# Kernel optimization log

Measured on AMD Instinct MI355X. Metric: run time of the kernel, lower is better.

The kernel has to match this reference:

```python
import jax, jax.numpy as jnp
import numpy as np

# Constants mirroring privacy_config
LEAK = 0.95          # membrane_leak_rate
REFR = 2.0           # refractory_period
SYN_EPS = 0.1        # synaptic_epsilon (threshold noise scale & privacy-cost factor)
NOISE_SCALE = 0.05   # spike_noise_scale on inputs
THRESH = 1.0         # spike_threshold init
SIZES = [1024, 2048, 1024, 512]
T, B = 16, 256


def setup_inputs() -> dict:
    key = jax.random.key(0)
    ks = jax.random.split(key, 16)
    inp = {"inputs": jax.random.normal(ks[0], (B, SIZES[0]), dtype=jnp.float32)}
    for i in range(3):
        nin, nout = SIZES[i], SIZES[i + 1]
        inp[f"w{i}"] = jax.random.normal(ks[1 + i], (nout, nin), dtype=jnp.float32) * 0.1
        inp[f"th{i}"] = jnp.full((nout,), THRESH, dtype=jnp.float32)
        inp[f"cn{i}"] = jax.random.normal(ks[4 + i], (T, B, nout), dtype=jnp.float32)
        inp[f"tn{i}"] = jax.random.normal(ks[7 + i], (T, B, nout), dtype=jnp.float32)
    inp["time_steps"] = T
    return inp


def _forward(inputs, ws, ths, cns, tns):
    # Vectorized leaky integrate-and-fire across (batch, neuron), scanned over time.
    Bsz = inputs.shape[0]
    Tn = cns[0].shape[0]
    nL = len(ws)
    V0 = tuple(jnp.zeros((Bsz, w.shape[0]), inputs.dtype) for w in ws)
    ls0 = tuple(jnp.full((Bsz, w.shape[0]), -1e9, inputs.dtype) for w in ws)  # last spike time
    wnorms = [jnp.linalg.norm(w, axis=1) for w in ws]  # per-neuron weight-vector norm [N]
    times = jnp.arange(1, Tn + 1, dtype=inputs.dtype)

    def step(carry, xs):
        t, cn_t, tn_t = xs
        Vs, ls = carry
        act = inputs  # input is re-presented at each time step (layer_activities[0])
        nV, nls, sps = [], [], []
        for i in range(nL):
            # per-neuron input noise ~ N(0, scale^2) dotted with w -> N(0, scale^2*||w||^2)
            cur = act @ ws[i].T + cn_t[i] * (NOISE_SCALE * wnorms[i])  # [B, N]
            refrac = (t - ls[i]) < REFR  # refractory neurons skip the update entirely
            Vn = jnp.where(refrac, Vs[i], LEAK * Vs[i] + cur)
            thr = ths[i] + tn_t[i] * SYN_EPS  # noisy privacy threshold
            sp = jnp.logical_and(jnp.logical_not(refrac), Vn > thr)
            nV.append(jnp.where(sp, 0.0, Vn))         # reset membrane on spike
            nls.append(jnp.where(sp, t, ls[i]))
            act = sp.astype(inputs.dtype)              # spikes feed next layer
            sps.append(act)
        return (tuple(nV), tuple(nls)), tuple(sps)

    _, spikes = jax.lax.scan(step, (V0, ls0), (times, tuple(cns), tuple(tns)))
    # spikes: tuple of [T, B, N_l] per layer

    # privacy cost: eps * (spikes in trailing 10-step window)/10 * ||w_neuron||, summed over all calls
    idx = jnp.arange(Tn)
    idx_hi = idx + 1
    idx_lo = jnp.clip(idx - 9, 0, Tn)
    cost = jnp.zeros((), inputs.dtype)
    tot = jnp.zeros((), inputs.dtype)
    cnt = 0
    for sp, wn in zip(spikes, wnorms):
        cs = jnp.concatenate([jnp.zeros_like(sp[:1]), jnp.cumsum(sp, axis=0)], axis=0)
        win = cs[idx_hi] - cs[idx_lo]  # [T, B, N] trailing-window spike counts
        cost = cost + SYN_EPS * jnp.sum(win / 10.0 * wn)
        tot = tot + jnp.sum(sp)
        cnt += sp.size
    # network entropy over the binary {0,1} spike pattern values
    p1 = tot / cnt
    p0 = 1.0 - p1
    eps = 1e-12
    entropy = -(p1 * jnp.log2(p1 + eps) + p0 * jnp.log2(p0 + eps))

    out = spikes[-1][-1]  # last layer activity at final time step, [B, N_last]
    return out, cost, entropy


def reference(inputs, w0, w1, w2, th0, th1, th2, cn0, cn1, cn2, tn0, tn1, tn2, time_steps):
    return _forward(inputs, (w0, w1, w2), (th0, th1, th2), (cn0, cn1, cn2), (tn0, tn1, tn2))
```

## Files before the change

kernel.cpp:

```cpp
#include <hip/hip_runtime.h>
#include <math.h>


#define T_STEPS 16

typedef short short8 __attribute__((ext_vector_type(8)));
typedef float floatx4 __attribute__((ext_vector_type(4)));

__device__ inline ushort f2bf(float x) {
  unsigned int u = __float_as_uint(x);
  unsigned int r = (u + 0x7FFFu + ((u >> 16) & 1u)) >> 16;
  return (ushort)r;
}
__device__ inline float bf2f(ushort h) {
  return __uint_as_float(((unsigned int)h) << 16);
}
__device__ inline floatx4 mfma16(short8 a, short8 b, floatx4 c) {
  return __builtin_amdgcn_mfma_f32_16x16x32_bf16(a, b, c, 0, 0, 0);
}

__device__ inline void gload16(const ushort* g, ushort* l) {
  __builtin_amdgcn_global_load_lds(
      (const __attribute__((address_space(1))) void*)g,
      (__attribute__((address_space(3))) void*)l, 16, 0, 0);
}

__device__ inline void stage_split16(const float* __restrict__ src, ushort* dsth, ushort* dstl) {
  float fv[16];
  #pragma unroll
  for (int i = 0; i < 4; ++i) *(float4*)&fv[4 * i] = *(const float4*)(src + 4 * i);
  unsigned int ph[8], pl[8];
  #pragma unroll
  for (int i = 0; i < 8; ++i) {
    ushort h0 = f2bf(fv[2 * i]);
    ushort l0 = f2bf(fv[2 * i] - bf2f(h0));
    ushort h1 = f2bf(fv[2 * i + 1]);
    ushort l1 = f2bf(fv[2 * i + 1] - bf2f(h1));
    ph[i] = (unsigned int)h0 | ((unsigned int)h1 << 16);
    pl[i] = (unsigned int)l0 | ((unsigned int)l1 << 16);
  }
  *(uint4*)dsth       = make_uint4(ph[0], ph[1], ph[2], ph[3]);
  *(uint4*)(dsth + 8) = make_uint4(ph[4], ph[5], ph[6], ph[7]);
  *(uint4*)dstl       = make_uint4(pl[0], pl[1], pl[2], pl[3]);
  *(uint4*)(dstl + 8) = make_uint4(pl[4], pl[5], pl[6], pl[7]);
}

__device__ inline void cost_store_bucket(float csum, int cnt, float2* __restrict__ cbuf,
                                         int bucket_base) {
  #pragma unroll
  for (int off = 32; off > 0; off >>= 1) {
    csum += __shfl_down(csum, off);
    cnt  += __shfl_down(cnt, off);
  }
  __shared__ float sc[4];
  __shared__ int   si[4];
  int wid = threadIdx.x >> 6;
  if ((threadIdx.x & 63) == 0) { sc[wid] = csum; si[wid] = cnt; }
  __syncthreads();
  if (threadIdx.x == 0) {
    float c = sc[0] + sc[1] + sc[2] + sc[3];
    int   k = si[0] + si[1] + si[2] + si[3];
    float2 v;
    v.x = c * 0.01f;
    v.y = (float)k;
    cbuf[bucket_base + blockIdx.x] = v;
  }
}


__global__ __launch_bounds__(64) void wnorm_kernel(const float* __restrict__ w0,
                                                   const float* __restrict__ w1,
                                                   const float* __restrict__ w2,
                                                   float* __restrict__ wn) {
  int r = blockIdx.x;
  const float* row; int K;
  if (r < 2048)      { row = w0 + (size_t)r * 1024;          K = 1024; }
  else if (r < 3072) { row = w1 + (size_t)(r - 2048) * 2048; K = 2048; }
  else               { row = w2 + (size_t)(r - 3072) * 1024; K = 1024; }
  float ss = 0.f;
  for (int k = threadIdx.x; k < K; k += 64) { float x = row[k]; ss += x * x; }
  #pragma unroll
  for (int off = 32; off > 0; off >>= 1) ss += __shfl_down(ss, off);
  if (threadIdx.x == 0) wn[r] = sqrtf(ss);
}


__global__ __launch_bounds__(256) void convert_w_kernel(const float* __restrict__ w1,
                                                        const float* __restrict__ w2,
                                                        ushort* __restrict__ w1b,
                                                        ushort* __restrict__ w2b) {
  int i = (blockIdx.x * 256 + threadIdx.x) * 8;
  const float* src; ushort* dst;
  if (i < 2097152) { src = w1 + i; dst = w1b + i; }
  else             { src = w2 + (i - 2097152); dst = w2b + (i - 2097152); }
  float4 a = *(const float4*)src;
  float4 b = *(const float4*)(src + 4);
  unsigned int p0 = (unsigned int)f2bf(a.x) | ((unsigned int)f2bf(a.y) << 16);
  unsigned int p1 = (unsigned int)f2bf(a.z) | ((unsigned int)f2bf(a.w) << 16);
  unsigned int p2 = (unsigned int)f2bf(b.x) | ((unsigned int)f2bf(b.y) << 16);
  unsigned int p3 = (unsigned int)f2bf(b.z) | ((unsigned int)f2bf(b.w) << 16);
  *(uint4*)dst = make_uint4(p0, p1, p2, p3);
}


__global__ __launch_bounds__(256) void base0_mfma_kernel(const float* __restrict__ A,
                                                         const float* __restrict__ W,
                                                         float* __restrict__ C) {
  __shared__ ushort Ah[64][72], Al[64][72], Bh[64][72], Bl[64][72];
  const int tid = threadIdx.x;
  const int m0 = blockIdx.x * 64;
  const int n0 = blockIdx.y * 64;
  const int lane = tid & 63, wv = tid >> 6;
  const int wm = wv & 1, wn2 = wv >> 1;
  const int l15 = lane & 15, quad = lane >> 4;
  const int sr = tid >> 2, scol = (tid & 3) * 16;

  floatx4 acc[2][2];
  #pragma unroll
  for (int i = 0; i < 2; ++i)
    #pragma unroll
    for (int j = 0; j < 2; ++j) acc[i][j] = (floatx4){0.f, 0.f, 0.f, 0.f};

  for (int k0 = 0; k0 < 1024; k0 += 64) {
    stage_split16(A + (size_t)(m0 + sr) * 1024 + k0 + scol, &Ah[sr][scol], &Al[sr][scol]);
    stage_split16(W + (size_t)(n0 + sr) * 1024 + k0 + scol, &Bh[sr][scol], &Bl[sr][scol]);
    __syncthreads();
    #pragma unroll
    for (int ks = 0; ks < 2; ++ks) {
      short8 ah[2], al[2], bh[2], bl[2];
      #pragma unroll
      for (int s = 0; s < 2; ++s) {
        ah[s] = *(const short8*)&Ah[32 * wm + 16 * s + l15][ks * 32 + quad * 8];
        al[s] = *(const short8*)&Al[32 * wm + 16 * s + l15][ks * 32 + quad * 8];
        bh[s] = *(const short8*)&Bh[32 * wn2 + 16 * s + l15][ks * 32 + quad * 8];
        bl[s] = *(const short8*)&Bl[32 * wn2 + 16 * s + l15][ks * 32 + quad * 8];
      }
      #pragma unroll
      for (int sm = 0; sm < 2; ++sm)
        #pragma unroll
        for (int sn = 0; sn < 2; ++sn) {
          acc[sm][sn] = mfma16(ah[sm], bh[sn], acc[sm][sn]);
          acc[sm][sn] = mfma16(ah[sm], bl[sn], acc[sm][sn]);
          acc[sm][sn] = mfma16(al[sm], bh[sn], acc[sm][sn]);
        }
    }
    __syncthreads();
  }
  #pragma unroll
  for (int sm = 0; sm < 2; ++sm)
    #pragma unroll
    for (int sn = 0; sn < 2; ++sn)
      #pragma unroll
      for (int r = 0; r < 4; ++r) {
        int m = m0 + 32 * wm + 16 * sm + quad * 4 + r;
        int n = n0 + 32 * wn2 + 16 * sn + l15;
        C[(size_t)m * 2048 + n] = acc[sm][sn][r];
      }
}


template<int K, int N, int NSPLIT>
__global__ __launch_bounds__(256) void gemm_lds_kernel(const ushort* __restrict__ A,
                                                       const ushort* __restrict__ W,
                                                       float* __restrict__ P) {
  __shared__ __attribute__((aligned(16))) ushort As[2][128 * 64];
  __shared__ __attribute__((aligned(16))) ushort Bs[2][128 * 64];
  constexpr int KS = K / NSPLIT;
  constexpr int NSTEP = KS / 64;
  constexpr int NT = N / 128;
  constexpr int MT = 32;
  constexpr int NWG = MT * NT * NSPLIT;

  const int orig = ((int)blockIdx.x % 8) * (NWG / 8) + (int)blockIdx.x / 8;
  const int sl = orig / (MT * NT);
  const int rem = orig % (MT * NT);
  const int m0 = (rem / NT) * 128;
  const int n0 = (rem % NT) * 128;

  const int tid = threadIdx.x;
  const int lane = tid & 63, wv = tid >> 6;
  const int wm = wv & 1, wn2 = wv >> 1;
  const int l15 = lane & 15, quad = lane >> 4;

  const ushort* Ab = A + (size_t)m0 * K + sl * KS;
  const ushort* Wb = W + (size_t)n0 * K + sl * KS;

  const int lrow = lane >> 3;
  const int lslot = (lane & 7) ^ lrow;

  floatx4 acc[4][4];
  #pragma unroll
  for (int i = 0; i < 4; ++i)
    #pragma unroll
    for (int j = 0; j < 4; ++j) acc[i][j] = (floatx4){0.f, 0.f, 0.f, 0.f};

  auto stage = [&](int buf, int k0) {
    #pragma unroll
    for (int h = 0; h < 4; ++h) {
      int r0 = wv * 32 + h * 8;
      const ushort* ga = Ab + (size_t)(r0 + lrow) * K + k0 + lslot * 8;
      const ushort* gb = Wb + (size_t)(r0 + lrow) * K + k0 + lslot * 8;
      gload16(ga, &As[buf][r0 * 64]);
      gload16(gb, &Bs[buf][r0 * 64]);
    }
  };
  auto compute = [&](int buf) {
    #pragma unroll
    for (int ks = 0; ks < 2; ++ks) {
      short8 af[4], bf[4];
      #pragma unroll
      for (int s = 0; s < 4; ++s) {
        int arow = wm * 64 + s * 16 + l15;
        int brow = wn2 * 64 + s * 16 + l15;
        af[s] = *(const short8*)&As[buf][arow * 64 + (((ks * 4 + quad) ^ (arow & 7)) << 3)];
        bf[s] = *(const short8*)&Bs[buf][brow * 64 + (((ks * 4 + quad) ^ (brow & 7)) << 3)];
      }
      #pragma unroll
      for (int sm = 0; sm < 4; ++sm)
        #pragma unroll
        for (int sn = 0; sn < 4; ++sn)
          acc[sm][sn] = mfma16(af[sm], bf[sn], acc[sm][sn]);
    }
  };

  stage(0, 0);
  __syncthreads();
  for (int kk = 0; kk < NSTEP; ++kk) {
    int buf = kk & 1;
    if (kk + 1 < NSTEP) stage(buf ^ 1, (kk + 1) * 64);
    compute(buf);
    __syncthreads();
  }

  float* Ps = P + (size_t)sl * 4096 * N;
  #pragma unroll
  for (int sm = 0; sm < 4; ++sm)
    #pragma unroll
    for (int sn = 0; sn < 4; ++sn)
      #pragma unroll
      for (int r = 0; r < 4; ++r) {
        int m = m0 + wm * 64 + sm * 16 + quad * 4 + r;
        int n = n0 + wn2 * 64 + sn * 16 + l15;
        Ps[(size_t)m * N + n] = acc[sm][sn][r];
      }
}


__global__ __launch_bounds__(256) void l0_lif_kernel(const float* __restrict__ base0,
                                                     const float* __restrict__ cn0,
                                                     const float* __restrict__ tn0,
                                                     const float* __restrict__ th0,
                                                     const float* __restrict__ wn0,
                                                     ushort* __restrict__ sp0,
                                                     float2* __restrict__ cbuf) {
  const int e = (blockIdx.x * 256 + threadIdx.x) * 4;
  const int n = e & 2047;
  float4 bb  = *(const float4*)(base0 + e);
  float4 th4 = *(const float4*)(th0 + n);
  float4 wn4 = *(const float4*)(wn0 + n);
  float bbv[4] = {bb.x, bb.y, bb.z, bb.w};
  float thv[4] = {th4.x, th4.y, th4.z, th4.w};
  float wnq[4] = {wn4.x, wn4.y, wn4.z, wn4.w};
  float V[4] = {0.f, 0.f, 0.f, 0.f};
  bool prev[4] = {false, false, false, false};
  float csum = 0.f; int cnt = 0;
  #pragma unroll 2
  for (int t = 1; t <= T_STEPS; ++t) {
    size_t off = (size_t)(t - 1) * 524288 + e;
    float4 c4 = *(const float4*)(cn0 + off);
    float4 t4 = *(const float4*)(tn0 + off);
    float cnv[4] = {c4.x, c4.y, c4.z, c4.w};
    float tnv[4] = {t4.x, t4.y, t4.z, t4.w};
    float f = (t <= 7) ? 10.f : (float)(17 - t);
    ushort sout[4];
    #pragma unroll
    for (int j = 0; j < 4; ++j) {
      float cur = bbv[j] + cnv[j] * (0.05f * wnq[j]);
      float Vn = prev[j] ? V[j] : (0.95f * V[j] + cur);
      float thr = thv[j] + tnv[j] * 0.1f;
      bool sp = (!prev[j]) && (Vn > thr);
      V[j] = sp ? 0.f : Vn;
      sout[j] = sp ? (ushort)0x3F80 : (ushort)0;
      prev[j] = sp;
      if (sp) { csum += wnq[j] * f; cnt++; }
    }
    ushort4 sq; sq.x = sout[0]; sq.y = sout[1]; sq.z = sout[2]; sq.w = sout[3];
    *(ushort4*)(sp0 + off) = sq;
  }
  cost_store_bucket(csum, cnt, cbuf, 0);
}


template<int N, bool LAST>
__global__ __launch_bounds__(256) void lif_seq_kernel(const float* __restrict__ P,
                                                      const float* __restrict__ cn,
                                                      const float* __restrict__ tn,
                                                      const float* __restrict__ th,
                                                      const float* __restrict__ wnv,
                                                      ushort* __restrict__ spout,
                                                      float* __restrict__ outF,
                                                      float2* __restrict__ cbuf,
                                                      int bucket_base) {
  constexpr int SZ = 256 * N;
  constexpr size_t SLICE = (size_t)16 * SZ;
  const int e = (blockIdx.x * 256 + threadIdx.x) * 4;
  const int n = e & (N - 1);
  float4 th4 = *(const float4*)(th + n);
  float4 wn4 = *(const float4*)(wnv + n);
  float thv[4] = {th4.x, th4.y, th4.z, th4.w};
  float wnq[4] = {wn4.x, wn4.y, wn4.z, wn4.w};
  float V[4] = {0.f, 0.f, 0.f, 0.f};
  bool prev[4] = {false, false, false, false};
  float csum = 0.f; int cnt = 0;
  #pragma unroll 2
  for (int t = 1; t <= T_STEPS; ++t) {
    size_t off = (size_t)(t - 1) * SZ + e;
    float4 p0 = *(const float4*)(P + off);
    float4 p1 = *(const float4*)(P + SLICE + off);
    float4 c4 = *(const float4*)(cn + off);
    float4 t4 = *(const float4*)(tn + off);
    float av[4]  = {p0.x + p1.x, p0.y + p1.y, p0.z + p1.z, p0.w + p1.w};
    float cnv[4] = {c4.x, c4.y, c4.z, c4.w};
    float tnv[4] = {t4.x, t4.y, t4.z, t4.w};
    float f = (t <= 7) ? 10.f : (float)(17 - t);
    ushort sout[4];
    #pragma unroll
    for (int j = 0; j < 4; ++j) {
      float cur = av[j] + cnv[j] * (0.05f * wnq[j]);
      float Vn = prev[j] ? V[j] : (0.95f * V[j] + cur);
      float thr = thv[j] + tnv[j] * 0.1f;
      bool sp = (!prev[j]) && (Vn > thr);
      V[j] = sp ? 0.f : Vn;
      sout[j] = sp ? (ushort)0x3F80 : (ushort)0;
      prev[j] = sp;
      if (sp) { csum += wnq[j] * f; cnt++; }
    }
    if (!LAST) {
      ushort4 sq; sq.x = sout[0]; sq.y = sout[1]; sq.z = sout[2]; sq.w = sout[3];
      *(ushort4*)(spout + off) = sq;
    } else if (t == T_STEPS) {
      *(float4*)(outF + e) = make_float4(sout[0] ? 1.f : 0.f, sout[1] ? 1.f : 0.f,
                                         sout[2] ? 1.f : 0.f, sout[3] ? 1.f : 0.f);
    }
  }
  cost_store_bucket(csum, cnt, cbuf, bucket_base);
}


__global__ __launch_bounds__(256) void finalize_kernel(const float2* __restrict__ cbuf,
                                                       float* __restrict__ out) {
  float c = 0.f, k = 0.f;
  for (int i = threadIdx.x; i < 896; i += 256) {
    float2 v = cbuf[i];
    c += v.x; k += v.y;
  }
  #pragma unroll
  for (int off = 32; off > 0; off >>= 1) {
    c += __shfl_down(c, off);
    k += __shfl_down(k, off);
  }
  __shared__ float sc[4], sk[4];
  int wid = threadIdx.x >> 6;
  if ((threadIdx.x & 63) == 0) { sc[wid] = c; sk[wid] = k; }
  __syncthreads();
  if (threadIdx.x == 0) {
    float cost = sc[0] + sc[1] + sc[2] + sc[3];
    float tot  = sk[0] + sk[1] + sk[2] + sk[3];
    float p1 = tot / 14680064.f;
    float p0 = 1.f - p1;
    float ent = -(p1 * log2f(p1 + 1e-12f) + p0 * log2f(p0 + 1e-12f));
    out[131072] = cost;
    out[131073] = ent;
  }
}


extern "C" void kernel_launch(void* const* d_in, const int* in_sizes, int n_in,
                              void* d_out, int out_size, void* d_ws, size_t ws_size,
                              hipStream_t stream) {
  const float* inputs = (const float*)d_in[0];
  const float* w0  = (const float*)d_in[1];
  const float* th0 = (const float*)d_in[2];
  const float* cn0 = (const float*)d_in[3];
  const float* tn0 = (const float*)d_in[4];
  const float* w1  = (const float*)d_in[5];
  const float* th1 = (const float*)d_in[6];
  const float* cn1 = (const float*)d_in[7];
  const float* tn1 = (const float*)d_in[8];
  const float* w2  = (const float*)d_in[9];
  const float* th2 = (const float*)d_in[10];
  const float* cn2 = (const float*)d_in[11];
  const float* tn2 = (const float*)d_in[12];
  float* out = (float*)d_out;
  float* ws  = (float*)d_ws;

  float* wn    = ws;
  float* base0 = ws + 4096;
  float* P1    = base0 + 524288;
  ushort* w1b  = (ushort*)(P1 + 8388608);
  ushort* w2b  = w1b + 2097152;
  ushort* sp0  = w2b + 524288;
  ushort* sp1  = sp0 + 8388608;
  float2* cbuf = (float2*)(sp1 + 4194304);
  float* P2    = (float*)sp0;

  wnorm_kernel<<<3584, 64, 0, stream>>>(w0, w1, w2, wn);
  convert_w_kernel<<<1280, 256, 0, stream>>>(w1, w2, w1b, w2b);
  base0_mfma_kernel<<<dim3(4, 32), 256, 0, stream>>>(inputs, w0, base0);

  l0_lif_kernel<<<512, 256, 0, stream>>>(base0, cn0, tn0, th0, wn, sp0, cbuf);

  gemm_lds_kernel<2048, 1024, 2><<<512, 256, 0, stream>>>(sp0, w1b, P1);

  lif_seq_kernel<1024, false><<<256, 256, 0, stream>>>(P1, cn1, tn1, th1, wn + 2048,
                                                       sp1, nullptr, cbuf, 512);

  gemm_lds_kernel<1024, 512, 2><<<256, 256, 0, stream>>>(sp1, w2b, P2);

  lif_seq_kernel<512, true><<<128, 256, 0, stream>>>(P2, cn2, tn2, th2, wn + 3072,
                                                     nullptr, out, cbuf, 768);

  finalize_kernel<<<1, 256, 0, stream>>>(cbuf, out);
}
```

Measured before the change: 294.8 us.

## Fuse layer GEMMs with LIF time scan using batch-major time-minor row layout

Spike matrices are reordered so each GEMM row block holds 16 time steps of 8 batch items. The LIF recurrence can then run directly on MFMA accumulators, with the membrane state chained across quads through lane shuffles. This removes the split-K partial-sum buffers, the separate LIF kernels, and the fp32 round trip through memory. The tiles shrink to 128x64 with no K split, and the noise loads in the epilogue are strided and uncoalesced, which may cost some efficiency in exchange.

```diff
diff --git a/kernel.cpp b/kernel.cpp
--- a/kernel.cpp
+++ b/kernel.cpp
@@ -159,66 +159,75 @@
 }
 
 
-template<int K, int N, int NSPLIT>
-__global__ __launch_bounds__(256) void gemm_lds_kernel(const ushort* __restrict__ A,
+template<int K, int N, bool LAST>
+__global__ __launch_bounds__(256) void gemm_lif_kernel(const ushort* __restrict__ A,
                                                        const ushort* __restrict__ W,
-                                                       float* __restrict__ P) {
+                                                       const float* __restrict__ cn,
+                                                       const float* __restrict__ tn,
+                                                       const float* __restrict__ th,
+                                                       const float* __restrict__ wnv,
+                                                       ushort* __restrict__ spout,
+                                                       float* __restrict__ outF,
+                                                       float2* __restrict__ cbuf,
+                                                       int bucket_base) {
   __shared__ __attribute__((aligned(16))) ushort As[2][128 * 64];
-  __shared__ __attribute__((aligned(16))) ushort Bs[2][128 * 64];
-  constexpr int KS = K / NSPLIT;
-  constexpr int NSTEP = KS / 64;
-  constexpr int NT = N / 128;
+  __shared__ __attribute__((aligned(16))) ushort Bs[2][64 * 64];
+  constexpr int NSTEP = K / 64;
+  constexpr int NT = N / 64;
   constexpr int MT = 32;
-  constexpr int NWG = MT * NT * NSPLIT;
+  constexpr int NWG = MT * NT;
 
   const int orig = ((int)blockIdx.x % 8) * (NWG / 8) + (int)blockIdx.x / 8;
-  const int sl = orig / (MT * NT);
-  const int rem = orig % (MT * NT);
-  const int m0 = (rem / NT) * 128;
-  const int n0 = (rem % NT) * 128;
+  const int m0 = (orig / NT) * 128;
+  const int n0 = (orig % NT) * 64;
 
   const int tid = threadIdx.x;
   const int lane = tid & 63, wv = tid >> 6;
   const int wm = wv & 1, wn2 = wv >> 1;
   const int l15 = lane & 15, quad = lane >> 4;
 
-  const ushort* Ab = A + (size_t)m0 * K + sl * KS;
-  const ushort* Wb = W + (size_t)n0 * K + sl * KS;
+  const ushort* Ab = A + (size_t)m0 * K;
+  const ushort* Wb = W + (size_t)n0 * K;
 
   const int lrow = lane >> 3;
   const int lslot = (lane & 7) ^ lrow;
 
-  floatx4 acc[4][4];
+  floatx4 acc[4][2];
   #pragma unroll
   for (int i = 0; i < 4; ++i)
     #pragma unroll
-    for (int j = 0; j < 4; ++j) acc[i][j] = (floatx4){0.f, 0.f, 0.f, 0.f};
+    for (int j = 0; j < 2; ++j) acc[i][j] = (floatx4){0.f, 0.f, 0.f, 0.f};
 
   auto stage = [&](int buf, int k0) {
     #pragma unroll
     for (int h = 0; h < 4; ++h) {
       int r0 = wv * 32 + h * 8;
-      const ushort* ga = Ab + (size_t)(r0 + lrow) * K + k0 + lslot * 8;
-      const ushort* gb = Wb + (size_t)(r0 + lrow) * K + k0 + lslot * 8;
-      gload16(ga, &As[buf][r0 * 64]);
-      gload16(gb, &Bs[buf][r0 * 64]);
+      gload16(Ab + (size_t)(r0 + lrow) * K + k0 + lslot * 8, &As[buf][r0 * 64]);
+    }
+    #pragma unroll
+    for (int h = 0; h < 2; ++h) {
+      int r0 = wv * 16 + h * 8;
+      gload16(Wb + (size_t)(r0 + lrow) * K + k0 + lslot * 8, &Bs[buf][r0 * 64]);
     }
   };
   auto compute = [&](int buf) {
     #pragma unroll
     for (int ks = 0; ks < 2; ++ks) {
-      short8 af[4], bf[4];
+      short8 af[4], bf[2];
       #pragma unroll
       for (int s = 0; s < 4; ++s) {
         int arow = wm * 64 + s * 16 + l15;
-        int brow = wn2 * 64 + s * 16 + l15;
         af[s] = *(const short8*)&As[buf][arow * 64 + (((ks * 4 + quad) ^ (arow & 7)) << 3)];
+      }
+      #pragma unroll
+      for (int s = 0; s < 2; ++s) {
+        int brow = wn2 * 32 + s * 16 + l15;
         bf[s] = *(const short8*)&Bs[buf][brow * 64 + (((ks * 4 + quad) ^ (brow & 7)) << 3)];
       }
       #pragma unroll
       for (int sm = 0; sm < 4; ++sm)
         #pragma unroll
-        for (int sn = 0; sn < 4; ++sn)
+        for (int sn = 0; sn < 2; ++sn)
           acc[sm][sn] = mfma16(af[sm], bf[sn], acc[sm][sn]);
     }
   };
@@ -232,17 +241,62 @@
     __syncthreads();
   }
 
-  float* Ps = P + (size_t)sl * 4096 * N;
-  #pragma unroll
-  for (int sm = 0; sm < 4; ++sm)
-    #pragma unroll
-    for (int sn = 0; sn < 4; ++sn)
+  float csum = 0.f; int cnt = 0;
+  #pragma unroll
+  for (int sm = 0; sm < 4; ++sm) {
+    const int b = (m0 >> 4) + wm * 4 + sm;
+    #pragma unroll
+    for (int sn = 0; sn < 2; ++sn) {
+      const int n = n0 + wn2 * 32 + sn * 16 + l15;
+      float cnv[4], tnv[4];
       #pragma unroll
       for (int r = 0; r < 4; ++r) {
-        int m = m0 + wm * 64 + sm * 16 + quad * 4 + r;
-        int n = n0 + wn2 * 64 + sn * 16 + l15;
-        Ps[(size_t)m * N + n] = acc[sm][sn][r];
-      }
+        size_t off = (size_t)(quad * 4 + r) * (256 * N) + (size_t)b * N + n;
+        cnv[r] = cn[off];
+        tnv[r] = tn[off];
+      }
+      const float thn = th[n];
+      const float wnn = wnv[n];
+      float V = 0.f; int prev = 0;
+      ushort skeep[4] = {0, 0, 0, 0};
+      #pragma unroll
+      for (int qq = 0; qq < 4; ++qq) {
+        float Vl = V; int pl = prev;
+        ushort slocal[4];
+        #pragma unroll
+        for (int r = 0; r < 4; ++r) {
+          float cur = acc[sm][sn][r] + cnv[r] * (0.05f * wnn);
+          float Vn = pl ? Vl : (0.95f * Vl + cur);
+          float thr = thn + tnv[r] * 0.1f;
+          bool sp = (!pl) && (Vn > thr);
+          Vl = sp ? 0.f : Vn;
+          slocal[r] = sp ? (ushort)0x3F80 : (ushort)0;
+          pl = sp ? 1 : 0;
+        }
+        if (quad == qq) {
+          #pragma unroll
+          for (int r = 0; r < 4; ++r) skeep[r] = slocal[r];
+        }
+        V = __shfl(Vl, l15 + (qq << 4));
+        prev = __shfl(pl, l15 + (qq << 4));
+      }
+      #pragma unroll
+      for (int r = 0; r < 4; ++r) {
+        int t = quad * 4 + r + 1;
+        float f = (t <= 7) ? 10.f : (float)(17 - t);
+        if (skeep[r]) { csum += wnn * f; cnt++; }
+      }
+      if (!LAST) {
+        const int mbase = m0 + wm * 64 + sm * 16 + quad * 4;
+        #pragma unroll
+        for (int r = 0; r < 4; ++r)
+          spout[(size_t)(mbase + r) * N + n] = skeep[r];
+      } else {
+        if (quad == 3) outF[(size_t)b * N + n] = skeep[3] ? 1.f : 0.f;
+      }
+    }
+  }
+  cost_store_bucket(csum, cnt, cbuf, bucket_base);
 }
 
 
@@ -255,6 +309,7 @@
                                                      float2* __restrict__ cbuf) {
   const int e = (blockIdx.x * 256 + threadIdx.x) * 4;
   const int n = e & 2047;
+  const int b = e >> 11;
   float4 bb  = *(const float4*)(base0 + e);
   float4 th4 = *(const float4*)(th0 + n);
   float4 wn4 = *(const float4*)(wn0 + n);
@@ -285,72 +340,16 @@
       if (sp) { csum += wnq[j] * f; cnt++; }
     }
     ushort4 sq; sq.x = sout[0]; sq.y = sout[1]; sq.z = sout[2]; sq.w = sout[3];
-    *(ushort4*)(sp0 + off) = sq;
+    *(ushort4*)(sp0 + (size_t)(b * 16 + t - 1) * 2048 + n) = sq;
   }
   cost_store_bucket(csum, cnt, cbuf, 0);
-}
-
-
-template<int N, bool LAST>
-__global__ __launch_bounds__(256) void lif_seq_kernel(const float* __restrict__ P,
-                                                      const float* __restrict__ cn,
-                                                      const float* __restrict__ tn,
-                                                      const float* __restrict__ th,
-                                                      const float* __restrict__ wnv,
-                                                      ushort* __restrict__ spout,
-                                                      float* __restrict__ outF,
-                                                      float2* __restrict__ cbuf,
-                                                      int bucket_base) {
-  constexpr int SZ = 256 * N;
-  constexpr size_t SLICE = (size_t)16 * SZ;
-  const int e = (blockIdx.x * 256 + threadIdx.x) * 4;
-  const int n = e & (N - 1);
-  float4 th4 = *(const float4*)(th + n);
-  float4 wn4 = *(const float4*)(wnv + n);
-  float thv[4] = {th4.x, th4.y, th4.z, th4.w};
-  float wnq[4] = {wn4.x, wn4.y, wn4.z, wn4.w};
-  float V[4] = {0.f, 0.f, 0.f, 0.f};
-  bool prev[4] = {false, false, false, false};
-  float csum = 0.f; int cnt = 0;
-  #pragma unroll 2
-  for (int t = 1; t <= T_STEPS; ++t) {
-    size_t off = (size_t)(t - 1) * SZ + e;
-    float4 p0 = *(const float4*)(P + off);
-    float4 p1 = *(const float4*)(P + SLICE + off);
-    float4 c4 = *(const float4*)(cn + off);
-    float4 t4 = *(const float4*)(tn + off);
-    float av[4]  = {p0.x + p1.x, p0.y + p1.y, p0.z + p1.z, p0.w + p1.w};
-    float cnv[4] = {c4.x, c4.y, c4.z, c4.w};
-    float tnv[4] = {t4.x, t4.y, t4.z, t4.w};
-    float f = (t <= 7) ? 10.f : (float)(17 - t);
-    ushort sout[4];
-    #pragma unroll
-    for (int j = 0; j < 4; ++j) {
-      float cur = av[j] + cnv[j] * (0.05f * wnq[j]);
-      float Vn = prev[j] ? V[j] : (0.95f * V[j] + cur);
-      float thr = thv[j] + tnv[j] * 0.1f;
-      bool sp = (!prev[j]) && (Vn > thr);
-      V[j] = sp ? 0.f : Vn;
-      sout[j] = sp ? (ushort)0x3F80 : (ushort)0;
-      prev[j] = sp;
-      if (sp) { csum += wnq[j] * f; cnt++; }
-    }
-    if (!LAST) {
-      ushort4 sq; sq.x = sout[0]; sq.y = sout[1]; sq.z = sout[2]; sq.w = sout[3];
-      *(ushort4*)(spout + off) = sq;
-    } else if (t == T_STEPS) {
-      *(float4*)(outF + e) = make_float4(sout[0] ? 1.f : 0.f, sout[1] ? 1.f : 0.f,
-                                         sout[2] ? 1.f : 0.f, sout[3] ? 1.f : 0.f);
-    }
-  }
-  cost_store_bucket(csum, cnt, cbuf, bucket_base);
 }
 
 
 __global__ __launch_bounds__(256) void finalize_kernel(const float2* __restrict__ cbuf,
                                                        float* __restrict__ out) {
   float c = 0.f, k = 0.f;
-  for (int i = threadIdx.x; i < 896; i += 256) {
+  for (int i = threadIdx.x; i < 1280; i += 256) {
     float2 v = cbuf[i];
     c += v.x; k += v.y;
   }
@@ -396,13 +395,11 @@
 
   float* wn    = ws;
   float* base0 = ws + 4096;
-  float* P1    = base0 + 524288;
-  ushort* w1b  = (ushort*)(P1 + 8388608);
+  ushort* w1b  = (ushort*)(base0 + 524288);
   ushort* w2b  = w1b + 2097152;
   ushort* sp0  = w2b + 524288;
   ushort* sp1  = sp0 + 8388608;
   float2* cbuf = (float2*)(sp1 + 4194304);
-  float* P2    = (float*)sp0;
 
   wnorm_kernel<<<3584, 64, 0, stream>>>(w0, w1, w2, wn);
   convert_w_kernel<<<1280, 256, 0, stream>>>(w1, w2, w1b, w2b);
@@ -410,15 +407,11 @@
 
   l0_lif_kernel<<<512, 256, 0, stream>>>(base0, cn0, tn0, th0, wn, sp0, cbuf);
 
-  gemm_lds_kernel<2048, 1024, 2><<<512, 256, 0, stream>>>(sp0, w1b, P1);
-
-  lif_seq_kernel<1024, false><<<256, 256, 0, stream>>>(P1, cn1, tn1, th1, wn + 2048,
-                                                       sp1, nullptr, cbuf, 512);
-
-  gemm_lds_kernel<1024, 512, 2><<<256, 256, 0, stream>>>(sp1, w2b, P2);
-
-  lif_seq_kernel<512, true><<<128, 256, 0, stream>>>(P2, cn2, tn2, th2, wn + 3072,
-                                                     nullptr, out, cbuf, 768);
+  gemm_lif_kernel<2048, 1024, false><<<512, 256, 0, stream>>>(
+      sp0, w1b, cn1, tn1, th1, wn + 2048, sp1, nullptr, cbuf, 512);
+
+  gemm_lif_kernel<1024, 512, true><<<256, 256, 0, stream>>>(
+      sp1, w2b, cn2, tn2, th2, wn + 3072, nullptr, out, cbuf, 1024);
 
   finalize_kernel<<<1, 256, 0, stream>>>(cbuf, out);
 }
```

Measured after the change: 290.9 us. About the same (-1.3%).
